# Optimization experiments

Hardware: AMD Instinct MI355X
Metric: run time of the kernel (lower is better)

The kernel has to match this reference:

```python
import jax, jax.numpy as jnp
import numpy as np
from jax import lax

B, NPB = 4, 100000
N = B * NPB
C_BEV, C = 256, 64
H = W = 180
S = 10          # NUM_SWEEPS
MAXI = 64       # gt_boxes.shape[1] (max instances per sample)
NUMLOC = B * MAXI * S
NUMINST = B * MAXI
PC_MIN = -54.0
CELL = 0.075 * 8  # voxel * bev_image_stride


def setup_inputs() -> dict:
    key = jax.random.key(0)
    ks = jax.random.split(key, 20)
    pb = jnp.repeat(jnp.arange(B), NPB).astype(jnp.float32)
    xy = jax.random.uniform(ks[0], (N, 2), minval=-54.0, maxval=53.9)
    z = jax.random.uniform(ks[1], (N, 1), minval=-5.0, maxval=2.9)
    extra = jax.random.uniform(ks[2], (N, 2))
    sweep = jax.random.randint(ks[3], (N, 1), 0, S).astype(jnp.float32)
    inst = jax.random.randint(ks[4], (N, 1), 0, MAXI).astype(jnp.float32)
    points = jnp.concatenate([pb[:, None], xy, z, extra, sweep, inst, inst], axis=1)
    sc = 0.05
    return {
        'points': points,
        'spatial_features_2d': jax.random.normal(ks[5], (B, C_BEV, H, W)),
        'conv_w': jax.random.normal(ks[6], (C, C_BEV, 3, 3)) * sc,
        'bn_gamma': jnp.ones((C,)), 'bn_beta': jnp.zeros((C,)),
        'w_seg': jax.random.normal(ks[7], (C, 3)) * sc, 'b_seg': jnp.zeros((3,)),
        'w_reg': jax.random.normal(ks[8], (C, 3)) * sc, 'b_reg': jnp.zeros((3,)),
        'w_emb': jax.random.normal(ks[9], (C, 2)) * sc, 'b_emb': jnp.zeros((2,)),
        'w_shape': jax.random.normal(ks[10], (3, C)) * sc, 'b_shape': jnp.zeros((C,)),
        'w_tf': jax.random.normal(ks[11], (2 * C + 6, 7)) * sc, 'b_tf': jnp.zeros((7,)),
        'w_mos': jax.random.normal(ks[12], (C + 6, 1)) * sc, 'b_mos': jnp.zeros((1,)),
    }


def _forward(points, spatial_features_2d, conv_w, bn_gamma, bn_beta,
             w_seg, b_seg, w_reg, b_reg, w_emb, b_emb,
             w_shape, b_shape, w_tf, b_tf, w_mos, b_mos):
    # ---- shared_conv: Conv3x3 (no bias) + BatchNorm2d (training stats) + ReLU
    y = lax.conv_general_dilated(spatial_features_2d, conv_w, (1, 1), 'SAME',
                                 dimension_numbers=('NCHW', 'OIHW', 'NCHW'))
    mu = y.mean(axis=(0, 2, 3), keepdims=True)
    var = y.var(axis=(0, 2, 3), keepdims=True)
    y = (y - mu) * lax.rsqrt(var + 1e-5)
    bev = jax.nn.relu(y * bn_gamma[None, :, None, None] + bn_beta[None, :, None, None])
    bev_hwc = jnp.transpose(bev, (0, 2, 3, 1))  # [B,H,W,C]

    # ---- bilinear gather of BEV features at point locations (vectorized over batch)
    pb = points[:, 0].astype(jnp.int32)
    px = (points[:, 1] - PC_MIN) / CELL
    py = (points[:, 2] - PC_MIN) / CELL
    x0 = jnp.clip(jnp.floor(px).astype(jnp.int32), 0, W - 1)
    x1 = jnp.clip(x0 + 1, 0, W - 1)
    y0 = jnp.clip(jnp.floor(py).astype(jnp.int32), 0, H - 1)
    y1 = jnp.clip(y0 + 1, 0, H - 1)
    x0f, x1f = x0.astype(px.dtype), x1.astype(px.dtype)
    y0f, y1f = y0.astype(py.dtype), y1.astype(py.dtype)
    Ia = bev_hwc[pb, y0, x0]
    Ib = bev_hwc[pb, y1, x0]
    Ic = bev_hwc[pb, y0, x1]
    Id = bev_hwc[pb, y1, x1]
    wa = ((x1f - px) * (y1f - py))[:, None]
    wb = ((x1f - px) * (py - y0f))[:, None]
    wc = ((px - x0f) * (y1f - py))[:, None]
    wd = ((px - x0f) * (py - y0f))[:, None]
    points_feat = Ia * wa + Ib * wb + Ic * wc + Id * wd  # [N, C]

    # ---- point heads (single Linear each, mid_c=None)
    points_cls_logit = points_feat @ w_seg + b_seg
    points_offset = points_feat @ w_reg + b_reg
    points_embedding = points_feat @ w_emb + b_emb

    # ---- instance / local aggregation (training branch; all points foreground)
    sweep = points[:, 6].astype(jnp.int32)
    inst = points[:, 7].astype(jnp.int32)
    seg = (pb * MAXI + inst) * S + sweep  # dense local id in [0, NUMLOC)
    cnt = jax.ops.segment_sum(jnp.ones((N,), points.dtype), seg, NUMLOC)
    nonempty = cnt > 0
    xyz = points[:, 1:4]
    centroid = jax.ops.segment_sum(xyz, seg, NUMLOC) / jnp.clip(cnt, 1.0)[:, None]
    centered = xyz - centroid[seg]

    shape_enc = jax.ops.segment_max(centered @ w_shape + b_shape, seg, NUMLOC)
    shape_enc = jnp.where(nonempty[:, None], shape_enc, 0.0)
    locals_feat = jax.ops.segment_max(points_feat, seg, NUMLOC)
    locals_feat = jnp.where(nonempty[:, None], locals_feat, 0.0)
    locals_feat = locals_feat + shape_enc  # [NUMLOC, C]

    inst_of_local = jnp.arange(NUMLOC, dtype=jnp.int32) // S
    sweep_of_local = jnp.arange(NUMLOC, dtype=jnp.int32) % S
    neg_inf = jnp.array(-jnp.inf, locals_feat.dtype)
    globals_feat = jax.ops.segment_max(
        jnp.where(nonempty[:, None], locals_feat, neg_inf), inst_of_local, NUMINST)
    inst_nonempty = jax.ops.segment_max(nonempty, inst_of_local, NUMINST)
    globals_feat = jnp.where(inst_nonempty[:, None], globals_feat, 0.0)

    max_sweep = jax.ops.segment_max(jnp.where(nonempty, sweep_of_local, -1), inst_of_local, NUMINST)
    min_sweep = jax.ops.segment_min(jnp.where(nonempty, sweep_of_local, S), inst_of_local, NUMINST)
    inst_ids = jnp.arange(NUMINST, dtype=jnp.int32)
    idx_max = jnp.clip(inst_ids * S + max_sweep, 0, NUMLOC - 1)
    idx_min = jnp.clip(inst_ids * S + min_sweep, 0, NUMLOC - 1)
    init_center = centroid[idx_min]    # [NUMINST, 3]
    target_center = centroid[idx_max]  # [NUMINST, 3]

    locals_cat = jnp.concatenate(
        [locals_feat, globals_feat[inst_of_local], centroid, target_center[inst_of_local]], axis=1)
    locals_tf = locals_cat @ w_tf + b_tf  # [NUMLOC, 7]
    inst_feat = jnp.concatenate([globals_feat, init_center, target_center], axis=1)
    inst_mos = inst_feat @ w_mos + b_mos  # [NUMINST, 1]

    return points_cls_logit, points_offset, points_embedding, locals_tf, inst_mos


def reference(points, spatial_features_2d, conv_w, bn_gamma, bn_beta,
              w_seg, b_seg, w_reg, b_reg, w_emb, b_emb,
              w_shape, b_shape, w_tf, b_tf, w_mos, b_mos):
    return _forward(points, spatial_features_2d, conv_w, bn_gamma, bn_beta,
                    w_seg, b_seg, w_reg, b_reg, w_emb, b_emb,
                    w_shape, b_shape, w_tf, b_tf, w_mos, b_mos)
```

## Files before the change

kernel.cpp:

```cpp
#include <hip/hip_runtime.h>

typedef __attribute__((ext_vector_type(8))) unsigned short u16x8;
typedef __attribute__((ext_vector_type(8))) short s16x8;
typedef __attribute__((ext_vector_type(4))) float f32x4;

#define NPTS 400000
#define HW 32400
#define WID 180
#define NCI 256
#define NCO 64
#define NSEG 2560
#define NINST 256
#define NBLK 500
#define PPB 800

__device__ __forceinline__ float bf2f(unsigned short u) {
  union { unsigned int i; float f; } v; v.i = ((unsigned int)u) << 16; return v.f;
}
__device__ __forceinline__ unsigned short f2bf(float f) {
  unsigned int u = __float_as_uint(f);
  return (unsigned short)((u + 0x7fffu + ((u >> 16) & 1u)) >> 16);
}

__device__ __forceinline__ void gld_lds16(const void* g, void* l) {
  __builtin_amdgcn_global_load_lds((const __attribute__((address_space(1))) void*)g,
                                   (__attribute__((address_space(3))) void*)l, 16, 0, 0);
}

__global__ __launch_bounds__(256) void k_transpose(const float* __restrict__ x,
                                                   unsigned short* __restrict__ xt) {
  const int bw = blockIdx.x;
  const int h = blockIdx.y, b = blockIdx.z;
  const int w0 = (bw >> 2) * 64, ci0 = (bw & 3) * 64;
  __shared__ float tile[64][68];
  const int t = threadIdx.x;
  const int a = t & 15, c4 = t >> 4;
  const int w4 = a * 4;
  const bool ldok = (w0 + w4) < WID;
#pragma unroll
  for (int it = 0; it < 4; ++it) {
    int ci = c4 + it * 16;
    float4 v = make_float4(0.f, 0.f, 0.f, 0.f);
    if (ldok) v = *(const float4*)(x + ((size_t)(b * NCI + ci0 + ci) * WID + h) * WID + w0 + w4);
    tile[w4 + 0][ci] = v.x;
    tile[w4 + 1][ci] = v.y;
    tile[w4 + 2][ci] = v.z;
    tile[w4 + 3][ci] = v.w;
  }
  __syncthreads();
  const int q = t & 7, r = t >> 3;
#pragma unroll
  for (int it = 0; it < 2; ++it) {
    int wl = r + it * 32;
    int w = w0 + wl;
    if (w >= WID) continue;
    const float* row = &tile[wl][q * 8];
    float4 lo = *(const float4*)(row);
    float4 hi = *(const float4*)(row + 4);
    u16x8 o;
    o[0] = f2bf(lo.x); o[1] = f2bf(lo.y); o[2] = f2bf(lo.z); o[3] = f2bf(lo.w);
    o[4] = f2bf(hi.x); o[5] = f2bf(hi.y); o[6] = f2bf(hi.z); o[7] = f2bf(hi.w);
    *(u16x8*)(xt + ((size_t)((b * WID + h) * WID + w)) * NCI + ci0 + q * 8) = o;
  }
}

__global__ void k_wreorg(const float* __restrict__ wt, unsigned short* __restrict__ wb) {
  int id = blockIdx.x * 256 + threadIdx.x;
  if (id >= 9 * 8 * 64 * 32) return;
  int cw = id & 31;
  int co = (id >> 5) & 63;
  int chunk = (id >> 11) & 7;
  int tap = id >> 14;
  int ci = chunk * 32 + cw;
  wb[id] = f2bf(wt[((size_t)co * 256 + ci) * 9 + tap]);
}

#define ROWB 6272
#define RBUF 25600
__global__ __launch_bounds__(256, 3) void k_conv_mfma(const unsigned short* __restrict__ xt,
                                                   const unsigned short* __restrict__ wb,
                                                   const float* __restrict__ zbuf,
                                                   unsigned short* __restrict__ y,
                                                   float* __restrict__ part) {
  const int wg = blockIdx.x;
  const int lin = (wg & 7) * 90 + (wg >> 3);
  const int h2 = lin % 90;
  const int t2 = lin / 90;
  const int wth = t2 & 1, b = t2 >> 1;
  const int h0 = h2 * 2;
  const int w0 = wth * 96;
  __shared__ unsigned char strip[2][RBUF];
  __shared__ float redS[2][2][2][16], redQ[2][2][2][16];
  const int tid = threadIdx.x;
  const int lane = tid & 63, wv = tid >> 6;
  const int mh = wv >> 1, nh = wv & 1;
  const int l15 = lane & 15, lk = lane >> 4;

  const char* srcs[7];
#pragma unroll
  for (int k = 0; k < 7; ++k) {
    int j = wv + k * 4;
    int g = j * 64 + lane;
    int pxlin = g >> 2, sub = g & 3;
    int row = pxlin / 98;
    int px = pxlin - row * 98;
    int hh = h0 + row - 1;
    int worig = w0 + px - 1;
    bool valid = (j < 25) && (pxlin < 392) &&
                 (hh >= 0) && (hh < WID) && (worig >= 0) && (worig < WID);
    int cig = sub ^ ((px >> 1) & 3);
    srcs[k] = valid
        ? (const char*)(xt + ((size_t)((b * WID + hh) * WID + worig)) * NCI + cig * 8)
        : (const char*)zbuf + lane * 16;
  }

  f32x4 acc[6][2];
#pragma unroll
  for (int i = 0; i < 6; ++i)
#pragma unroll
    for (int j = 0; j < 2; ++j) { acc[i][j][0] = 0.f; acc[i][j][1] = 0.f; acc[i][j][2] = 0.f; acc[i][j][3] = 0.f; }

  auto stage = [&](unsigned char* buf, int chunk) {
#pragma unroll
    for (int k = 0; k < 7; ++k) {
      int j = wv + k * 4;
      if (j >= 25) break;
      gld_lds16(srcs[k] + chunk * 64, buf + j * 1024);
    }
  };

  stage(strip[0], 0);
  asm volatile("s_waitcnt vmcnt(0)" ::: "memory");
  __syncthreads();

  const unsigned short* wco[2];
#pragma unroll
  for (int nf = 0; nf < 2; ++nf)
    wco[nf] = wb + (size_t)((nh * 2 + nf) * 16 + l15) * 32 + lk * 8;

  for (int chunk = 0; chunk < 8; ++chunk) {
    s16x8 bfr[9][2];
#pragma unroll
    for (int tap = 0; tap < 9; ++tap)
#pragma unroll
      for (int nf = 0; nf < 2; ++nf)
        bfr[tap][nf] = *(const s16x8*)(wco[nf] + (size_t)(tap * 8 + chunk) * 2048);
    if (chunk < 7) stage(strip[(chunk + 1) & 1], chunk + 1);
    const unsigned char* buf = strip[chunk & 1];
#pragma unroll
    for (int tap = 0; tap < 9; ++tap) {
      const int dh = tap / 3, dw = tap % 3;
      s16x8 afr[6];
#pragma unroll
      for (int i = 0; i < 6; ++i) {
        int wp = i * 16 + l15 + dw;
        int byte = (mh + dh) * ROWB + wp * 64 + ((lk ^ ((wp >> 1) & 3)) * 16);
        afr[i] = *(const s16x8*)(buf + byte);
      }
#pragma unroll
      for (int i = 0; i < 6; ++i)
#pragma unroll
        for (int nf = 0; nf < 2; ++nf)
          acc[i][nf] = __builtin_amdgcn_mfma_f32_16x16x32_bf16(afr[i], bfr[tap][nf], acc[i][nf], 0, 0, 0);
    }
    asm volatile("s_waitcnt vmcnt(0)" ::: "memory");
    __syncthreads();
  }

  const int r4 = lk * 4;
  const int hrow = h0 + mh;
  float s[2] = {0.f, 0.f}, q[2] = {0.f, 0.f};
#pragma unroll
  for (int i = 0; i < 6; ++i) {
#pragma unroll
    for (int nf = 0; nf < 2; ++nf) {
      int co = (nh * 2 + nf) * 16 + l15;
#pragma unroll
      for (int j = 0; j < 4; ++j) {
        int w = w0 + i * 16 + r4 + j;
        if (w < WID) {
          float v = acc[i][nf][j];
          y[((size_t)(b * HW) + hrow * WID + w) * 64 + co] = f2bf(v);
          s[nf] += v; q[nf] = fmaf(v, v, q[nf]);
        }
      }
    }
  }
#pragma unroll
  for (int nf = 0; nf < 2; ++nf) {
    s[nf] += __shfl_xor(s[nf], 16); s[nf] += __shfl_xor(s[nf], 32);
    q[nf] += __shfl_xor(q[nf], 16); q[nf] += __shfl_xor(q[nf], 32);
  }
  if (lk == 0) {
#pragma unroll
    for (int nf = 0; nf < 2; ++nf) { redS[mh][nh][nf][l15] = s[nf]; redQ[mh][nh][nf][l15] = q[nf]; }
  }
  __syncthreads();
  if (tid < 64) {
    int co = tid;
    int nhh = co >> 5, nff = (co >> 4) & 1, ll = co & 15;
    part[((size_t)wg * 64 + co) * 2 + 0] = redS[0][nhh][nff][ll] + redS[1][nhh][nff][ll];
    part[((size_t)wg * 64 + co) * 2 + 1] = redQ[0][nhh][nff][ll] + redQ[1][nhh][nff][ll];
  }
}

__global__ void k_bnparams(const float* __restrict__ part, const float* __restrict__ gamma,
                           const float* __restrict__ beta, float* __restrict__ ab) {
  const int t = threadIdx.x;
  float s = 0.f, ss = 0.f;
  for (int k = 0; k < 720; ++k) { s += part[((size_t)k * 64 + t) * 2]; ss += part[((size_t)k * 64 + t) * 2 + 1]; }
  float mu = s / 129600.f;
  float var = ss / 129600.f - mu * mu;
  float a = rsqrtf(var + 1e-5f) * gamma[t];
  ab[t * 2] = a; ab[t * 2 + 1] = beta[t] - mu * a;
}

__global__ __launch_bounds__(256) void k_points(const float* __restrict__ pts,
                         const unsigned short* __restrict__ y,
                         const float* __restrict__ ab,
                         unsigned short* __restrict__ pf) {
  const int gid = blockIdx.x * 256 + threadIdx.x;
  const int lane = gid & 63;
  const int wid = gid >> 6;
  const float sa = ab[lane * 2], sb = ab[lane * 2 + 1];
#pragma unroll
  for (int it = 0; it < 4; ++it) {
    int p = wid * 4 + it;
    const float* pr = pts + (size_t)p * 9;
    float pbf = pr[0], xx = pr[1], yy = pr[2];
    int b = (int)pbf;
    float px = (xx - (-54.0f)) / 0.6f;
    float py = (yy - (-54.0f)) / 0.6f;
    int x0 = (int)floorf(px); x0 = min(max(x0, 0), WID - 1);
    int x1 = min(x0 + 1, WID - 1);
    int y0 = (int)floorf(py); y0 = min(max(y0, 0), WID - 1);
    int y1 = min(y0 + 1, WID - 1);
    float x0f = (float)x0, x1f = (float)x1, y0f = (float)y0, y1f = (float)y1;
    float wa = (x1f - px) * (y1f - py);
    float wb = (x1f - px) * (py - y0f);
    float wc = (px - x0f) * (y1f - py);
    float wd = (px - x0f) * (py - y0f);
    int i00 = y0 * WID + x0;
    int dx = x1 - x0;
    int dy = (y1 - y0) * WID;
    const unsigned short* bb = y + ((size_t)b * HW) * 64 + lane;
    float Ia = fmaf(bf2f(bb[(size_t)i00 * 64]), sa, sb);            Ia = Ia > 0.f ? Ia : 0.f;
    float Ic = fmaf(bf2f(bb[(size_t)(i00 + dx) * 64]), sa, sb);     Ic = Ic > 0.f ? Ic : 0.f;
    float Ib = fmaf(bf2f(bb[(size_t)(i00 + dy) * 64]), sa, sb);     Ib = Ib > 0.f ? Ib : 0.f;
    float Id = fmaf(bf2f(bb[(size_t)(i00 + dy + dx) * 64]), sa, sb); Id = Id > 0.f ? Id : 0.f;
    float f = wa * Ia + wb * Ib + wc * Ic + wd * Id;
    pf[(size_t)p * 64 + lane] = f2bf(f);
  }
}

__global__ void k_heads(const unsigned short* __restrict__ pf,
                        const float* __restrict__ wseg, const float* __restrict__ bseg,
                        const float* __restrict__ wreg, const float* __restrict__ breg,
                        const float* __restrict__ wemb, const float* __restrict__ bemb,
                        float* __restrict__ ocls, float* __restrict__ ooff, float* __restrict__ oemb) {
  const int p = blockIdx.x * 256 + threadIdx.x;
  if (p >= NPTS) return;
  float a0 = bseg[0], a1 = bseg[1], a2 = bseg[2];
  float r0 = breg[0], r1 = breg[1], r2 = breg[2];
  float e0 = bemb[0], e1 = bemb[1];
  const u16x8* q = (const u16x8*)(pf + (size_t)p * 64);
#pragma unroll
  for (int g = 0; g < 8; ++g) {
    u16x8 v8 = q[g];
#pragma unroll
    for (int k = 0; k < 8; ++k) {
      int kk = g * 8 + k;
      float v = bf2f(v8[k]);
      a0 = fmaf(v, wseg[kk * 3 + 0], a0);
      a1 = fmaf(v, wseg[kk * 3 + 1], a1);
      a2 = fmaf(v, wseg[kk * 3 + 2], a2);
      r0 = fmaf(v, wreg[kk * 3 + 0], r0);
      r1 = fmaf(v, wreg[kk * 3 + 1], r1);
      r2 = fmaf(v, wreg[kk * 3 + 2], r2);
      e0 = fmaf(v, wemb[kk * 2 + 0], e0);
      e1 = fmaf(v, wemb[kk * 2 + 1], e1);
    }
  }
  ocls[p * 3 + 0] = a0; ocls[p * 3 + 1] = a1; ocls[p * 3 + 2] = a2;
  ooff[p * 3 + 0] = r0; ooff[p * 3 + 1] = r1; ooff[p * 3 + 2] = r2;
  oemb[p * 2 + 0] = e0; oemb[p * 2 + 1] = e1;
}

__global__ __launch_bounds__(256) void k_hist2(const float* __restrict__ pts,
                                               int* __restrict__ seg, int* __restrict__ rankp,
                                               int* __restrict__ bh) {
  __shared__ int lc[NSEG];
  const int t = threadIdx.x, blk = blockIdx.x;
  for (int i = t; i < NSEG; i += 256) lc[i] = 0;
  __syncthreads();
  const int p0 = blk * PPB;
  for (int i = t; i < PPB; i += 256) {
    int p = p0 + i;
    const float* pr = pts + (size_t)p * 9;
    int b = (int)pr[0];
    int sw = (int)pr[6];
    int ins = (int)pr[7];
    int s = (b * 64 + ins) * 10 + sw;
    seg[p] = s;
    rankp[p] = atomicAdd(&lc[s], 1);
  }
  __syncthreads();
  for (int i = t; i < NSEG; i += 256) bh[i * NBLK + blk] = lc[i];
}

__global__ void k_scan2a(const int* __restrict__ bh, int* __restrict__ basebk,
                         int* __restrict__ tot) {
  const int s = blockIdx.x * 256 + threadIdx.x;
  const int4* row = (const int4*)(bh + (size_t)s * NBLK);
  int4* brow = (int4*)(basebk + (size_t)s * NBLK);
  int acc = 0;
  for (int b = 0; b < NBLK / 4; ++b) {
    int4 v = row[b];
    int4 o;
    o.x = acc; acc += v.x;
    o.y = acc; acc += v.y;
    o.z = acc; acc += v.z;
    o.w = acc; acc += v.w;
    brow[b] = o;
  }
  tot[s] = acc;
}

__global__ void k_scan2b(const int* __restrict__ tot, int* __restrict__ base,
                         int* __restrict__ cnt) {
  __shared__ int csum[256];
  const int t = threadIdx.x;
  int loc[10]; int run = 0;
#pragma unroll
  for (int k = 0; k < 10; ++k) { loc[k] = tot[t * 10 + k]; run += loc[k]; }
  csum[t] = run;
  __syncthreads();
  if (t == 0) {
    int a = 0;
    for (int i = 0; i < 256; ++i) { int v = csum[i]; csum[i] = a; a += v; }
  }
  __syncthreads();
  int acc = csum[t];
#pragma unroll
  for (int k = 0; k < 10; ++k) {
    int s = t * 10 + k;
    base[s] = acc; cnt[s] = loc[k];
    acc += loc[k];
  }
}

__global__ void k_scatter2(const int* __restrict__ seg, const int* __restrict__ rankp,
                           const int* __restrict__ base, const int* __restrict__ basebk,
                           int* __restrict__ order) {
  const int p = blockIdx.x * 256 + threadIdx.x;
  if (p < NPTS) {
    int s = seg[p];
    int blk = p / PPB;
    order[base[s] + basebk[s * NBLK + blk] + rankp[p]] = p;
  }
}

__global__ __launch_bounds__(256) void k_seg(const int* __restrict__ cnt, const int* __restrict__ base,
                      const int* __restrict__ order, const float* __restrict__ pts,
                      const unsigned short* __restrict__ pf,
                      const float* __restrict__ wsh, const float* __restrict__ bsh,
                      float* __restrict__ lf, float* __restrict__ centroid,
                      int* __restrict__ nonempty) {
  const int s = blockIdx.x;
  const int t = threadIdx.x, lane = t & 63, wv = t >> 6;
  const int n = cnt[s], bs = base[s];
  float sx = 0.f, sy = 0.f, sz = 0.f;
  for (int i = t; i < n; i += 256) {
    int p = order[bs + i];
    const float* pr = pts + (size_t)p * 9;
    sx += pr[1]; sy += pr[2]; sz += pr[3];
  }
#pragma unroll
  for (int m = 32; m > 0; m >>= 1) {
    sx += __shfl_xor(sx, m); sy += __shfl_xor(sy, m); sz += __shfl_xor(sz, m);
  }
  __shared__ float red[3][4];
  __shared__ float csh[3];
  if (lane == 0) { red[0][wv] = sx; red[1][wv] = sy; red[2][wv] = sz; }
  __syncthreads();
  if (t == 0) {
    float dn = (float)max(n, 1);
    csh[0] = (red[0][0] + red[0][1] + red[0][2] + red[0][3]) / dn;
    csh[1] = (red[1][0] + red[1][1] + red[1][2] + red[1][3]) / dn;
    csh[2] = (red[2][0] + red[2][1] + red[2][2] + red[2][3]) / dn;
  }
  __syncthreads();
  const float cx = csh[0], cy = csh[1], cz = csh[2];
  const float w0 = wsh[lane], w1 = wsh[64 + lane], w2 = wsh[128 + lane], bb = bsh[lane];
  float smax = -INFINITY, lmax = -INFINITY;
  for (int i = wv; i < n; i += 4) {
    int p = order[bs + i];
    const float* pr = pts + (size_t)p * 9;
    float sv = fmaf(pr[1] - cx, w0, fmaf(pr[2] - cy, w1, fmaf(pr[3] - cz, w2, bb)));
    smax = fmaxf(smax, sv);
    lmax = fmaxf(lmax, bf2f(pf[(size_t)p * 64 + lane]));
  }
  __shared__ float rs[4][64], rl[4][64];
  rs[wv][lane] = smax; rl[wv][lane] = lmax;
  __syncthreads();
  if (wv == 0) {
    smax = fmaxf(fmaxf(rs[0][lane], rs[1][lane]), fmaxf(rs[2][lane], rs[3][lane]));
    lmax = fmaxf(fmaxf(rl[0][lane], rl[1][lane]), fmaxf(rl[2][lane], rl[3][lane]));
    bool ne = n > 0;
    lf[s * 64 + lane] = (ne ? lmax : 0.f) + (ne ? smax : 0.f);
    if (lane == 0) {
      nonempty[s] = ne ? 1 : 0;
      centroid[s * 3 + 0] = cx; centroid[s * 3 + 1] = cy; centroid[s * 3 + 2] = cz;
    }
  }
}

__global__ void k_glob(const float* __restrict__ lf, const int* __restrict__ ne,
                       const float* __restrict__ centroid,
                       const float* __restrict__ wmos, const float* __restrict__ bmos,
                       float* __restrict__ gf, float* __restrict__ tc, float* __restrict__ ic,
                       float* __restrict__ omos) {
  const int i = blockIdx.x;
  const int t = threadIdx.x;
  float g = -INFINITY;
  int maxsw = -1, minsw = 10;
  bool any = false;
#pragma unroll
  for (int s = 0; s < 10; ++s) {
    int idx = i * 10 + s;
    bool e = ne[idx] != 0;
    float v = lf[idx * 64 + t];
    g = fmaxf(g, e ? v : -INFINITY);
    if (e) { any = true; maxsw = s; minsw = min(minsw, s); }
  }
  float gv = any ? g : 0.f;
  gf[i * 64 + t] = gv;
  int idxmax = min(max(i * 10 + maxsw, 0), NSEG - 1);
  int idxmin = min(max(i * 10 + minsw, 0), NSEG - 1);
  float tcx = centroid[idxmax * 3 + 0], tcy = centroid[idxmax * 3 + 1], tcz = centroid[idxmax * 3 + 2];
  float icx = centroid[idxmin * 3 + 0], icy = centroid[idxmin * 3 + 1], icz = centroid[idxmin * 3 + 2];
  if (t == 0) {
    tc[i * 3 + 0] = tcx; tc[i * 3 + 1] = tcy; tc[i * 3 + 2] = tcz;
    ic[i * 3 + 0] = icx; ic[i * 3 + 1] = icy; ic[i * 3 + 2] = icz;
  }
  float r = gv * wmos[t];
#pragma unroll
  for (int m = 32; m > 0; m >>= 1) r += __shfl_xor(r, m);
  if (t == 0) {
    r += icx * wmos[64] + icy * wmos[65] + icz * wmos[66];
    r += tcx * wmos[67] + tcy * wmos[68] + tcz * wmos[69];
    omos[i] = r + bmos[0];
  }
}

__global__ void k_tf(const float* __restrict__ lf, const float* __restrict__ gf,
                     const float* __restrict__ centroid, const float* __restrict__ tc,
                     const float* __restrict__ wtf, const float* __restrict__ btf,
                     float* __restrict__ otf) {
  const int r = blockIdx.x * 256 + threadIdx.x;
  if (r >= NSEG) return;
  const int i = r / 10;
  float acc[7];
#pragma unroll
  for (int j = 0; j < 7; ++j) acc[j] = btf[j];
  for (int k = 0; k < 64; ++k) {
    float v = lf[r * 64 + k];
#pragma unroll
    for (int j = 0; j < 7; ++j) acc[j] = fmaf(v, wtf[k * 7 + j], acc[j]);
  }
  for (int k = 0; k < 64; ++k) {
    float v = gf[i * 64 + k];
#pragma unroll
    for (int j = 0; j < 7; ++j) acc[j] = fmaf(v, wtf[(64 + k) * 7 + j], acc[j]);
  }
#pragma unroll
  for (int c = 0; c < 3; ++c) {
    float v = centroid[r * 3 + c];
#pragma unroll
    for (int j = 0; j < 7; ++j) acc[j] = fmaf(v, wtf[(128 + c) * 7 + j], acc[j]);
  }
#pragma unroll
  for (int c = 0; c < 3; ++c) {
    float v = tc[i * 3 + c];
#pragma unroll
    for (int j = 0; j < 7; ++j) acc[j] = fmaf(v, wtf[(131 + c) * 7 + j], acc[j]);
  }
#pragma unroll
  for (int j = 0; j < 7; ++j) otf[r * 7 + j] = acc[j];
}

extern "C" void kernel_launch(void* const* d_in, const int* in_sizes, int n_in,
                              void* d_out, int out_size, void* d_ws, size_t ws_size,
                              hipStream_t stream) {
  const float* pts   = (const float*)d_in[0];
  const float* x     = (const float*)d_in[1];
  const float* convw = (const float*)d_in[2];
  const float* gamma = (const float*)d_in[3];
  const float* beta  = (const float*)d_in[4];
  const float* wseg  = (const float*)d_in[5];
  const float* bseg  = (const float*)d_in[6];
  const float* wreg  = (const float*)d_in[7];
  const float* breg  = (const float*)d_in[8];
  const float* wemb  = (const float*)d_in[9];
  const float* bemb  = (const float*)d_in[10];
  const float* wsh   = (const float*)d_in[11];
  const float* bsh   = (const float*)d_in[12];
  const float* wtf   = (const float*)d_in[13];
  const float* btf   = (const float*)d_in[14];
  const float* wmos  = (const float*)d_in[15];
  const float* bmos  = (const float*)d_in[16];

  float* out = (float*)d_out;
  float* o_cls = out;
  float* o_off = out + 1200000;
  float* o_emb = out + 2400000;
  float* o_tf  = out + 3200000;
  float* o_mos = out + 3217920;

  char* wsp = (char*)d_ws;
  size_t off = 0;
  auto alloc = [&](size_t bytes) -> void* {
    void* p = wsp + off;
    off = (off + bytes + 255) & ~(size_t)255;
    return p;
  };
  unsigned short* xt   = (unsigned short*)alloc((size_t)4 * WID * WID * NCI * 2);
  unsigned short* pf   = xt;
  unsigned short* wbuf = (unsigned short*)alloc((size_t)9 * 8 * 64 * 32 * 2);
  unsigned short* y    = (unsigned short*)alloc((size_t)4 * HW * 64 * 2);
  int*   seg      = (int*)alloc((size_t)NPTS * 4);
  int*   rankp    = (int*)alloc((size_t)NPTS * 4);
  int*   order    = (int*)alloc((size_t)NPTS * 4);
  int*   bh       = (int*)alloc((size_t)NSEG * NBLK * 4);
  int*   basebk   = (int*)alloc((size_t)NSEG * NBLK * 4);
  int*   tot      = (int*)alloc(NSEG * 4);
  int*   cnt      = (int*)alloc(NSEG * 4);
  int*   base     = (int*)alloc(NSEG * 4);
  float* part     = (float*)alloc((size_t)720 * 64 * 2 * 4);
  float* ab       = (float*)alloc(64 * 2 * 4);
  float* centroid = (float*)alloc(NSEG * 3 * 4);
  float* lf       = (float*)alloc(NSEG * 64 * 4);
  int*   nonem    = (int*)alloc(NSEG * 4);
  float* gf       = (float*)alloc(NINST * 64 * 4);
  float* tc       = (float*)alloc(NINST * 3 * 4);
  float* ic       = (float*)alloc(NINST * 3 * 4);
  float* zbuf     = (float*)alloc(2048);
  (void)ws_size; (void)n_in; (void)in_sizes; (void)out_size;

  hipMemsetAsync(zbuf, 0, 2048, stream);

  k_hist2<<<NBLK, 256, 0, stream>>>(pts, seg, rankp, bh);
  k_scan2a<<<10, 256, 0, stream>>>(bh, basebk, tot);
  k_scan2b<<<1, 256, 0, stream>>>(tot, base, cnt);
  k_scatter2<<<(NPTS + 255) / 256, 256, 0, stream>>>(seg, rankp, base, basebk, order);
  k_transpose<<<dim3(12, WID, 4), 256, 0, stream>>>(x, xt);
  k_wreorg<<<576, 256, 0, stream>>>(convw, wbuf);
  k_conv_mfma<<<720, 256, 0, stream>>>(xt, wbuf, zbuf, y, part);
  k_bnparams<<<1, 64, 0, stream>>>(part, gamma, beta, ab);
  k_points<<<25000, 256, 0, stream>>>(pts, y, ab, pf);
  k_heads<<<(NPTS + 255) / 256, 256, 0, stream>>>(pf, wseg, bseg, wreg, breg, wemb, bemb,
                                                  o_cls, o_off, o_emb);
  k_seg<<<NSEG, 256, 0, stream>>>(cnt, base, order, pts, pf, wsh, bsh, lf, centroid, nonem);
  k_glob<<<NINST, 64, 0, stream>>>(lf, nonem, centroid, wmos, bmos, gf, tc, ic, o_mos);
  k_tf<<<(NSEG + 255) / 256, 256, 0, stream>>>(lf, gf, centroid, tc, wtf, btf, o_tf);
}
```

Before: 327.8 us.

## Fuse point heads into bilinear sampling kernel and transpose block histogram layout

The per-point seg/reg/emb linear heads are folded into k_points. Sampled features are staged in shared memory and 128 threads each compute one output per point from fp32 values, so k_heads and its re-read of pf disappear. The block histogram is stored block-major, so histogram writes and the per-segment scan become coalesced across threads instead of strided rows. The heads now use unrounded fp32 features rather than bf16-rounded ones, which changes results slightly, and the fused kernel adds a block barrier.

```diff
diff --git a/kernel.cpp b/kernel.cpp
--- a/kernel.cpp
+++ b/kernel.cpp
@@ -218,10 +218,22 @@
 __global__ __launch_bounds__(256) void k_points(const float* __restrict__ pts,
                          const unsigned short* __restrict__ y,
                          const float* __restrict__ ab,
-                         unsigned short* __restrict__ pf) {
-  const int gid = blockIdx.x * 256 + threadIdx.x;
-  const int lane = gid & 63;
-  const int wid = gid >> 6;
+                         const float* __restrict__ wseg, const float* __restrict__ bseg,
+                         const float* __restrict__ wreg, const float* __restrict__ breg,
+                         const float* __restrict__ wemb, const float* __restrict__ bemb,
+                         unsigned short* __restrict__ pf,
+                         float* __restrict__ ocls, float* __restrict__ ooff,
+                         float* __restrict__ oemb) {
+  __shared__ float fsh[16][66];
+  __shared__ float wsh2[512];
+  const int t = threadIdx.x;
+#pragma unroll
+  for (int e = t; e < 512; e += 256) {
+    int k = e >> 3, j = e & 7;
+    wsh2[e] = j < 3 ? wseg[k * 3 + j] : (j < 6 ? wreg[k * 3 + (j - 3)] : wemb[k * 2 + (j - 6)]);
+  }
+  const int lane = t & 63, wv = t >> 6;
+  const int wid = blockIdx.x * 4 + wv;
   const float sa = ab[lane * 2], sb = ab[lane * 2 + 1];
 #pragma unroll
   for (int it = 0; it < 4; ++it) {
@@ -244,46 +256,26 @@
     int dx = x1 - x0;
     int dy = (y1 - y0) * WID;
     const unsigned short* bb = y + ((size_t)b * HW) * 64 + lane;
-    float Ia = fmaf(bf2f(bb[(size_t)i00 * 64]), sa, sb);            Ia = Ia > 0.f ? Ia : 0.f;
-    float Ic = fmaf(bf2f(bb[(size_t)(i00 + dx) * 64]), sa, sb);     Ic = Ic > 0.f ? Ic : 0.f;
-    float Ib = fmaf(bf2f(bb[(size_t)(i00 + dy) * 64]), sa, sb);     Ib = Ib > 0.f ? Ib : 0.f;
+    float Ia = fmaf(bf2f(bb[(size_t)i00 * 64]), sa, sb);             Ia = Ia > 0.f ? Ia : 0.f;
+    float Ic = fmaf(bf2f(bb[(size_t)(i00 + dx) * 64]), sa, sb);      Ic = Ic > 0.f ? Ic : 0.f;
+    float Ib = fmaf(bf2f(bb[(size_t)(i00 + dy) * 64]), sa, sb);      Ib = Ib > 0.f ? Ib : 0.f;
     float Id = fmaf(bf2f(bb[(size_t)(i00 + dy + dx) * 64]), sa, sb); Id = Id > 0.f ? Id : 0.f;
     float f = wa * Ia + wb * Ib + wc * Ic + wd * Id;
     pf[(size_t)p * 64 + lane] = f2bf(f);
-  }
-}
-
-__global__ void k_heads(const unsigned short* __restrict__ pf,
-                        const float* __restrict__ wseg, const float* __restrict__ bseg,
-                        const float* __restrict__ wreg, const float* __restrict__ breg,
-                        const float* __restrict__ wemb, const float* __restrict__ bemb,
-                        float* __restrict__ ocls, float* __restrict__ ooff, float* __restrict__ oemb) {
-  const int p = blockIdx.x * 256 + threadIdx.x;
-  if (p >= NPTS) return;
-  float a0 = bseg[0], a1 = bseg[1], a2 = bseg[2];
-  float r0 = breg[0], r1 = breg[1], r2 = breg[2];
-  float e0 = bemb[0], e1 = bemb[1];
-  const u16x8* q = (const u16x8*)(pf + (size_t)p * 64);
-#pragma unroll
-  for (int g = 0; g < 8; ++g) {
-    u16x8 v8 = q[g];
-#pragma unroll
-    for (int k = 0; k < 8; ++k) {
-      int kk = g * 8 + k;
-      float v = bf2f(v8[k]);
-      a0 = fmaf(v, wseg[kk * 3 + 0], a0);
-      a1 = fmaf(v, wseg[kk * 3 + 1], a1);
-      a2 = fmaf(v, wseg[kk * 3 + 2], a2);
-      r0 = fmaf(v, wreg[kk * 3 + 0], r0);
-      r1 = fmaf(v, wreg[kk * 3 + 1], r1);
-      r2 = fmaf(v, wreg[kk * 3 + 2], r2);
-      e0 = fmaf(v, wemb[kk * 2 + 0], e0);
-      e1 = fmaf(v, wemb[kk * 2 + 1], e1);
-    }
-  }
-  ocls[p * 3 + 0] = a0; ocls[p * 3 + 1] = a1; ocls[p * 3 + 2] = a2;
-  ooff[p * 3 + 0] = r0; ooff[p * 3 + 1] = r1; ooff[p * 3 + 2] = r2;
-  oemb[p * 2 + 0] = e0; oemb[p * 2 + 1] = e1;
+    fsh[wv * 4 + it][lane] = f;
+  }
+  __syncthreads();
+  if (t < 128) {
+    int pt = t >> 3, j = t & 7;
+    int p = blockIdx.x * 16 + pt;
+    float acc = j < 3 ? bseg[j] : (j < 6 ? breg[j - 3] : bemb[j - 6]);
+    const float* row = fsh[pt];
+#pragma unroll
+    for (int k = 0; k < 64; ++k) acc = fmaf(row[k], wsh2[k * 8 + j], acc);
+    if (j < 3)      ocls[p * 3 + j] = acc;
+    else if (j < 6) ooff[p * 3 + (j - 3)] = acc;
+    else            oemb[p * 2 + (j - 6)] = acc;
+  }
 }
 
 __global__ __launch_bounds__(256) void k_hist2(const float* __restrict__ pts,
@@ -305,23 +297,17 @@
     rankp[p] = atomicAdd(&lc[s], 1);
   }
   __syncthreads();
-  for (int i = t; i < NSEG; i += 256) bh[i * NBLK + blk] = lc[i];
+  for (int i = t; i < NSEG; i += 256) bh[(size_t)blk * NSEG + i] = lc[i];
 }
 
 __global__ void k_scan2a(const int* __restrict__ bh, int* __restrict__ basebk,
                          int* __restrict__ tot) {
   const int s = blockIdx.x * 256 + threadIdx.x;
-  const int4* row = (const int4*)(bh + (size_t)s * NBLK);
-  int4* brow = (int4*)(basebk + (size_t)s * NBLK);
   int acc = 0;
-  for (int b = 0; b < NBLK / 4; ++b) {
-    int4 v = row[b];
-    int4 o;
-    o.x = acc; acc += v.x;
-    o.y = acc; acc += v.y;
-    o.z = acc; acc += v.z;
-    o.w = acc; acc += v.w;
-    brow[b] = o;
+  for (int b = 0; b < NBLK; ++b) {
+    int v = bh[(size_t)b * NSEG + s];
+    basebk[(size_t)b * NSEG + s] = acc;
+    acc += v;
   }
   tot[s] = acc;
 }
@@ -356,7 +342,7 @@
   if (p < NPTS) {
     int s = seg[p];
     int blk = p / PPB;
-    order[base[s] + basebk[s * NBLK + blk] + rankp[p]] = p;
+    order[base[s] + basebk[(size_t)blk * NSEG + s] + rankp[p]] = p;
   }
 }
 
@@ -531,8 +517,8 @@
   int*   seg      = (int*)alloc((size_t)NPTS * 4);
   int*   rankp    = (int*)alloc((size_t)NPTS * 4);
   int*   order    = (int*)alloc((size_t)NPTS * 4);
-  int*   bh       = (int*)alloc((size_t)NSEG * NBLK * 4);
-  int*   basebk   = (int*)alloc((size_t)NSEG * NBLK * 4);
+  int*   bh       = (int*)alloc((size_t)NBLK * NSEG * 4);
+  int*   basebk   = (int*)alloc((size_t)NBLK * NSEG * 4);
   int*   tot      = (int*)alloc(NSEG * 4);
   int*   cnt      = (int*)alloc(NSEG * 4);
   int*   base     = (int*)alloc(NSEG * 4);
@@ -557,9 +543,8 @@
   k_wreorg<<<576, 256, 0, stream>>>(convw, wbuf);
   k_conv_mfma<<<720, 256, 0, stream>>>(xt, wbuf, zbuf, y, part);
   k_bnparams<<<1, 64, 0, stream>>>(part, gamma, beta, ab);
-  k_points<<<25000, 256, 0, stream>>>(pts, y, ab, pf);
-  k_heads<<<(NPTS + 255) / 256, 256, 0, stream>>>(pf, wseg, bseg, wreg, breg, wemb, bemb,
-                                                  o_cls, o_off, o_emb);
+  k_points<<<25000, 256, 0, stream>>>(pts, y, ab, wseg, bseg, wreg, breg, wemb, bemb,
+                                      pf, o_cls, o_off, o_emb);
   k_seg<<<NSEG, 256, 0, stream>>>(cnt, base, order, pts, pf, wsh, bsh, lf, centroid, nonem);
   k_glob<<<NINST, 64, 0, stream>>>(lf, nonem, centroid, wmos, bmos, gf, tc, ic, o_mos);
   k_tf<<<(NSEG + 255) / 256, 256, 0, stream>>>(lf, gf, centroid, tc, wtf, btf, o_tf);
```

After: 341.7 us. +4.2%, slower.
